# Performance work log

Measured on AMD Instinct MI355X. Metric: run time of the kernel, lower is better.

Reference implementation:

```python
import jax, jax.numpy as jnp
import numpy as np

N = 50000
E = 800000
IN_C = 128
HID = 256
OUT_C = 51


def graph_conv(x, edge_index, edge_weight, w_rel, b_rel, w_root):
    # PyG GraphConv: out = lin_rel(aggr_add(w_e * x_src)) + lin_root(x)
    src, dst = edge_index[0], edge_index[1]
    msgs = x[src] * edge_weight[:, None]            # [E, F]
    agg = jax.ops.segment_sum(msgs, dst, num_segments=x.shape[0])  # [N, F]
    return agg @ w_rel + b_rel + x @ w_root


def setup_inputs() -> dict:
    key = jax.random.key(0)
    ks = jax.random.split(key, 10)
    s = lambda fan_in: 1.0 / np.sqrt(fan_in)
    return {
        "x0": jax.random.normal(ks[0], (N, IN_C), jnp.float32),
        "edge_index": jax.random.randint(ks[1], (2, E), 0, N, jnp.int64),
        "edge_weight": jax.random.uniform(ks[2], (E,), jnp.float32),
        "conv1_w_rel": jax.random.uniform(ks[3], (IN_C, HID), jnp.float32, -s(IN_C), s(IN_C)),
        "conv1_b_rel": jnp.zeros((HID,), jnp.float32),
        "conv1_w_root": jax.random.uniform(ks[4], (IN_C, HID), jnp.float32, -s(IN_C), s(IN_C)),
        "conv2_w_rel": jax.random.uniform(ks[5], (HID, HID), jnp.float32, -s(HID), s(HID)),
        "conv2_b_rel": jnp.zeros((HID,), jnp.float32),
        "conv2_w_root": jax.random.uniform(ks[6], (HID, HID), jnp.float32, -s(HID), s(HID)),
        "lin_w": jax.random.uniform(ks[7], (2 * HID, OUT_C), jnp.float32, -s(2 * HID), s(2 * HID)),
        "lin_b": jnp.zeros((OUT_C,), jnp.float32),
    }


def reference(x0, edge_index, edge_weight,
              conv1_w_rel, conv1_b_rel, conv1_w_root,
              conv2_w_rel, conv2_b_rel, conv2_w_root,
              lin_w, lin_b):
    # eval mode: dropout is identity
    x1 = jax.nn.relu(graph_conv(x0, edge_index, edge_weight, conv1_w_rel, conv1_b_rel, conv1_w_root))
    x2 = jax.nn.relu(graph_conv(x1, edge_index, edge_weight, conv2_w_rel, conv2_b_rel, conv2_w_root))
    x = jnp.concatenate([x1, x2], axis=-1)          # [N, 2H]
    return x @ lin_w + lin_b                         # [N, OUT_C]
```

## Files before the change

kernel.cpp:

```cpp
#include <hip/hip_runtime.h>
#include <hip/hip_bf16.h>

#define N_NODES 50000
#define N_EDGES 800000
#define IN_CH   128
#define HID     256
#define OUTC    51

typedef __attribute__((ext_vector_type(8))) short  bf16x8;
typedef __attribute__((ext_vector_type(4))) float  f32x4;
typedef __attribute__((ext_vector_type(2))) float  f32x2;
typedef __attribute__((ext_vector_type(4))) unsigned int u32x4;

__device__ __forceinline__ float bf2f(unsigned short u) {
    union { unsigned int i; float f; } v; v.i = ((unsigned int)u) << 16; return v.f;
}
__device__ __forceinline__ unsigned short f2bf(float f) {
    union { float f; unsigned int i; } v; v.f = f;
    unsigned int u = v.i;
    unsigned int r = (u + 0x7fffu + ((u >> 16) & 1u)) >> 16;
    return (unsigned short)r;
}
__device__ __forceinline__ unsigned short ldbf(const void* p, long i, int isf) {
    return isf ? f2bf(((const float*)p)[i]) : ((const unsigned short*)p)[i];
}
__device__ __forceinline__ float ldf(const void* p, long i, int isf) {
    return isf ? ((const float*)p)[i] : bf2f(((const unsigned short*)p)[i]);
}
__device__ __forceinline__ void load_edge_nt(const int* __restrict__ ei, int e, int is64,
                                             int* src, int* dst) {
    if (is64) { *src = __builtin_nontemporal_load(ei + 2 * e);
                *dst = __builtin_nontemporal_load(ei + 2 * (N_EDGES + e)); }
    else      { *src = __builtin_nontemporal_load(ei + e);
                *dst = __builtin_nontemporal_load(ei + N_EDGES + e); }
}

#define EBLK 1024
#define HB   ((N_EDGES + EBLK - 1) / EBLK)
#define NBKT ((N_NODES + 255) / 256)

__global__ __launch_bounds__(256) void init_kernel(const unsigned int* __restrict__ x0w,
                                                   int* __restrict__ flags,
                                                   const int* __restrict__ ei) {
    int tid = threadIdx.x;
    if (blockIdx.x == 0) {
        if (tid < 64) {
            unsigned int w = x0w[tid];
            unsigned int ex = (w >> 7) & 0xFFu;
            unsigned long long bm = __ballot(ex >= 0x60u && ex <= 0x90u);
            if (tid == 0) flags[0] = (__popcll(bm) >= 48) ? 0 : 1;
        }
        return;
    }
    __shared__ int any;
    if (tid == 0) any = 0;
    __syncthreads();
    int acc = 0;
    for (int s = 0; s < 8; s++) {
        int i = (tid * 8 + s) * (N_EDGES / 2048);
        acc |= ei[2 * i + 1];
    }
    if (acc != 0) any = 1;
    __syncthreads();
    if (tid == 0) flags[1] = any;
}

__global__ void prep_all_kernel(const void* __restrict__ x0, int cb,
                                const void* __restrict__ w1r, const void* __restrict__ w1x,
                                const void* __restrict__ w2r, const void* __restrict__ w2x,
                                const void* __restrict__ lw,
                                const void* __restrict__ b1h, const void* __restrict__ b2h,
                                const void* __restrict__ lbh, const int* __restrict__ flags,
                                unsigned short* __restrict__ x0bf,
                                unsigned short* __restrict__ Bt1, unsigned short* __restrict__ Bt2,
                                unsigned short* __restrict__ Bt3,
                                float* __restrict__ b1, float* __restrict__ b2, float* __restrict__ b3) {
    int isf = flags[0];
    if ((int)blockIdx.x < cb) {
        if (!isf) return;
        long t = (long)blockIdx.x * 256 + threadIdx.x;
        if (t < (long)N_NODES * IN_CH) x0bf[t] = f2bf(((const float*)x0)[t]);
        return;
    }
    int t = (blockIdx.x - cb) * 256 + threadIdx.x;
    if (t < 256 * 256) {
        int n = t >> 8, k = t & 255;
        Bt1[n * 256 + k] = (k < 128) ? ldbf(w1r, k * 256 + n, isf) : ldbf(w1x, (k - 128) * 256 + n, isf);
        return;
    }
    t -= 256 * 256;
    if (t < 256 * 512) {
        int n = t >> 9, k = t & 511;
        Bt2[n * 512 + k] = (k < 256) ? ldbf(w2r, k * 256 + n, isf) : ldbf(w2x, (k - 256) * 256 + n, isf);
        return;
    }
    t -= 256 * 512;
    if (t < 64 * 512) {
        int n = t >> 9, k = t & 511;
        Bt3[n * 512 + k] = (n < OUTC) ? ldbf(lw, k * OUTC + n, isf) : (unsigned short)0;
        return;
    }
    t -= 64 * 512;
    if (t < 256) { b1[t] = ldf(b1h, t, isf); return; }
    t -= 256;
    if (t < 256) { b2[t] = ldf(b2h, t, isf); return; }
    t -= 256;
    if (t < 64)  { b3[t] = (t < OUTC) ? ldf(lbh, t, isf) : 0.0f; return; }
}

__global__ __launch_bounds__(256) void h1_kernel(const int* __restrict__ ei, const int* __restrict__ flags,
                                                 unsigned int* __restrict__ bc) {
    __shared__ unsigned int cnt[NBKT];
    int tid = threadIdx.x;
    if (tid < NBKT) cnt[tid] = 0;
    __syncthreads();
    int is64 = (flags[1] == 0);
    int e0 = blockIdx.x * EBLK;
#pragma unroll
    for (int u = 0; u < 4; u++) {
        int e = e0 + u * 256 + tid;
        if (e < N_EDGES) {
            int src, dst; load_edge_nt(ei, e, is64, &src, &dst);
            if ((unsigned)src < N_NODES && (unsigned)dst < N_NODES)
                atomicAdd(&cnt[dst >> 8], 1u);
        }
    }
    __syncthreads();
    if (tid < NBKT) bc[tid * HB + blockIdx.x] = cnt[tid];
}

__global__ __launch_bounds__(1024) void s1_kernel(const unsigned int* __restrict__ bc,
                                                  unsigned int* __restrict__ pbase,
                                                  unsigned int* __restrict__ total) {
    __shared__ unsigned int sd[1024];
    int b = blockIdx.x, tid = threadIdx.x;
    unsigned int v = (tid < HB) ? bc[b * HB + tid] : 0u;
    sd[tid] = v;
    __syncthreads();
    for (int off = 1; off < 1024; off <<= 1) {
        unsigned int t = (tid >= off) ? sd[tid - off] : 0u;
        __syncthreads();
        sd[tid] += t;
        __syncthreads();
    }
    if (tid < HB) pbase[tid * NBKT + b] = sd[tid] - v;
    if (tid == 1023) total[b] = sd[1023];
}

__global__ __launch_bounds__(256) void s2_kernel(const unsigned int* __restrict__ total,
                                                 unsigned int* __restrict__ bbase,
                                                 int* __restrict__ rp) {
    __shared__ unsigned int sd[256];
    int tid = threadIdx.x;
    unsigned int v = (tid < NBKT) ? total[tid] : 0u;
    sd[tid] = v;
    __syncthreads();
    for (int off = 1; off < 256; off <<= 1) {
        unsigned int t = (tid >= off) ? sd[tid - off] : 0u;
        __syncthreads();
        sd[tid] += t;
        __syncthreads();
    }
    if (tid < NBKT) bbase[tid] = sd[tid] - v;
    if (tid == NBKT - 1) { bbase[NBKT] = sd[tid]; rp[N_NODES] = (int)sd[tid]; }
}

__global__ __launch_bounds__(256) void f1_kernel(const int* __restrict__ ei, const void* __restrict__ ew,
                                                 const int* __restrict__ flags,
                                                 const unsigned int* __restrict__ pbase,
                                                 const unsigned int* __restrict__ bbase,
                                                 uint2* __restrict__ rec) {
    __shared__ unsigned int cur[NBKT];
    int tid = threadIdx.x;
    if (tid < NBKT) cur[tid] = bbase[tid] + pbase[blockIdx.x * NBKT + tid];
    __syncthreads();
    int is64 = (flags[1] == 0);
    int isf = flags[0];
    int e0 = blockIdx.x * EBLK;
#pragma unroll
    for (int u = 0; u < 4; u++) {
        int e = e0 + u * 256 + tid;
        if (e < N_EDGES) {
            int src, dst; load_edge_nt(ei, e, is64, &src, &dst);
            if ((unsigned)src < N_NODES && (unsigned)dst < N_NODES) {
                unsigned int w = ldbf(ew, e, isf);
                unsigned int pos = atomicAdd(&cur[dst >> 8], 1u);
                uint2 r; r.x = (w << 16) | (unsigned)src; r.y = (unsigned)dst;
                rec[pos] = r;
            }
        }
    }
}

__global__ __launch_bounds__(512) void f2_kernel(const uint2* __restrict__ rec,
                                                 const unsigned int* __restrict__ bbase,
                                                 int* __restrict__ rp, unsigned int* __restrict__ cw) {
    __shared__ unsigned int c2[256], sc[256], cur2[256];
    int tid = threadIdx.x, b = blockIdx.x;
    unsigned int s0 = bbase[b], e0 = bbase[b + 1];
    if (tid < 256) c2[tid] = 0;
    __syncthreads();
    for (unsigned int pos = s0 + tid; pos < e0; pos += 512)
        atomicAdd(&c2[rec[pos].y & 255u], 1u);
    __syncthreads();
    unsigned int v = 0;
    if (tid < 256) { v = c2[tid]; sc[tid] = v; }
    __syncthreads();
    for (int off = 1; off < 256; off <<= 1) {
        unsigned int t = (tid < 256 && tid >= off) ? sc[tid - off] : 0u;
        __syncthreads();
        if (tid < 256) sc[tid] += t;
        __syncthreads();
    }
    if (tid < 256) {
        unsigned int start = s0 + sc[tid] - v;
        int node = b * 256 + tid;
        if (node < N_NODES) rp[node] = (int)start;
        cur2[tid] = start;
    }
    __syncthreads();
    for (unsigned int pos = s0 + tid; pos < e0; pos += 512) {
        uint2 r = rec[pos];
        unsigned int p = atomicAdd(&cur2[r.y & 255u], 1u);
        cw[p] = r.x;
    }
}

__global__ __launch_bounds__(256) void zout_kernel(unsigned short* __restrict__ out, long n) {
    long t = (long)blockIdx.x * 256 + threadIdx.x;
    if (t < n) out[t] = 0;
}

__global__ __launch_bounds__(256) void x1f8_kernel(const unsigned short* __restrict__ X12,
                                                   unsigned char* __restrict__ x1f8,
                                                   const int* __restrict__ flags, int f8mode) {
    int usef8 = (f8mode == 2) || (f8mode == 1 && flags[0] == 0);
    if (!usef8) return;
    int t = blockIdx.x * 256 + threadIdx.x;
    if (t >= N_NODES * 32) return;
    int row = t >> 5, c8 = (t & 31) * 8;
    u32x4 v = *(const u32x4*)(X12 + (long)row * 512 + c8);
    float f0 = bf2f((unsigned short)(v[0] & 0xffffu)), f1 = bf2f((unsigned short)(v[0] >> 16));
    float f2 = bf2f((unsigned short)(v[1] & 0xffffu)), f3 = bf2f((unsigned short)(v[1] >> 16));
    float f4 = bf2f((unsigned short)(v[2] & 0xffffu)), f5 = bf2f((unsigned short)(v[2] >> 16));
    float f6 = bf2f((unsigned short)(v[3] & 0xffffu)), f7 = bf2f((unsigned short)(v[3] >> 16));
    int lo = 0, hi = 0;
    lo = __builtin_amdgcn_cvt_pk_fp8_f32(f0, f1, lo, false);
    lo = __builtin_amdgcn_cvt_pk_fp8_f32(f2, f3, lo, true);
    hi = __builtin_amdgcn_cvt_pk_fp8_f32(f4, f5, hi, false);
    hi = __builtin_amdgcn_cvt_pk_fp8_f32(f6, f7, hi, true);
    uint2 pk; pk.x = (unsigned int)lo; pk.y = (unsigned int)hi;
    *(uint2*)(x1f8 + (long)row * 256 + c8) = pk;
}

__global__ __launch_bounds__(256) void agg1_kernel(const unsigned short* __restrict__ x0raw,
                                                   const unsigned short* __restrict__ x0conv,
                                                   int use_conv, const int* __restrict__ flags,
                                                   const int* __restrict__ rp, const unsigned int* __restrict__ cw,
                                                   unsigned short* __restrict__ X12) {
    const unsigned short* x0b = (use_conv && flags[0]) ? x0conv : x0raw;
    int r = blockIdx.x * 8 + (threadIdx.x >> 5);
    if (r >= N_NODES) return;
    int l = threadIdx.x & 31;
    int grpbase = threadIdx.x & 32;
    int js = rp[r], je = rp[r + 1];
    if (js < 0) js = 0;
    if (je > N_EDGES) je = N_EDGES;
    const uint2* xw = (const uint2*)x0b;
    float a0 = 0.f, a1 = 0.f, a2 = 0.f, a3 = 0.f;
    for (int base = js; base < je; base += 32) {
        int n = je - base; if (n > 32) n = 32;
        int idx = base + l; if (idx >= je) idx = je - 1;
        unsigned int rec = __builtin_nontemporal_load(cw + idx);
        for (int j = 0; j < n; j += 8) {
            int m = n - j; if (m > 8) m = 8;
            unsigned int vv[8]; uint2 q[8];
#pragma unroll
            for (int u = 0; u < 8; u++) vv[u] = __shfl(rec, grpbase + j + u);
#pragma unroll
            for (int u = 0; u < 8; u++) if (u < m)
                q[u] = xw[(long)(vv[u] & 0xFFFFu) * 32 + l];
#pragma unroll
            for (int u = 0; u < 8; u++) if (u < m) {
                float w = bf2f((unsigned short)(vv[u] >> 16));
                a0 += w * bf2f((unsigned short)(q[u].x & 0xffffu));
                a1 += w * bf2f((unsigned short)(q[u].x >> 16));
                a2 += w * bf2f((unsigned short)(q[u].y & 0xffffu));
                a3 += w * bf2f((unsigned short)(q[u].y >> 16));
            }
        }
    }
    uint2 pk;
    pk.x = (unsigned int)f2bf(a0) | ((unsigned int)f2bf(a1) << 16);
    pk.y = (unsigned int)f2bf(a2) | ((unsigned int)f2bf(a3) << 16);
    *(uint2*)&X12[(long)r * 512 + 256 + l * 4] = pk;
}

__global__ __launch_bounds__(256) void agg2_kernel(const int* __restrict__ rp, const unsigned int* __restrict__ cw,
                                                   unsigned short* __restrict__ X12,
                                                   const unsigned char* __restrict__ x1f8,
                                                   const int* __restrict__ flags, int f8mode) {
    int usef8 = (f8mode == 2) || (f8mode == 1 && flags[0] == 0);
    int r = blockIdx.x * 8 + (threadIdx.x >> 5);
    if (r >= N_NODES) return;
    int l = threadIdx.x & 31;
    int grpbase = threadIdx.x & 32;
    int js = rp[r], je = rp[r + 1];
    if (js < 0) js = 0;
    if (je > N_EDGES) je = N_EDGES;
    float a0 = 0.f, a1 = 0.f, a2 = 0.f, a3 = 0.f;
    float a4 = 0.f, a5 = 0.f, a6 = 0.f, a7 = 0.f;
    if (usef8) {
        for (int base = js; base < je; base += 32) {
            int n = je - base; if (n > 32) n = 32;
            int idx = base + l; if (idx >= je) idx = je - 1;
            unsigned int rec = __builtin_nontemporal_load(cw + idx);
            for (int j = 0; j < n; j += 8) {
                int m = n - j; if (m > 8) m = 8;
                unsigned int vv[8]; uint2 q[8];
#pragma unroll
                for (int u = 0; u < 8; u++) vv[u] = __shfl(rec, grpbase + j + u);
#pragma unroll
                for (int u = 0; u < 8; u++) if (u < m)
                    q[u] = *(const uint2*)(x1f8 + (long)(vv[u] & 0xFFFFu) * 256 + l * 8);
#pragma unroll
                for (int u = 0; u < 8; u++) if (u < m) {
                    float w = bf2f((unsigned short)(vv[u] >> 16));
                    f32x2 p0 = __builtin_amdgcn_cvt_pk_f32_fp8((int)q[u].x, false);
                    f32x2 p1 = __builtin_amdgcn_cvt_pk_f32_fp8((int)q[u].x, true);
                    f32x2 p2 = __builtin_amdgcn_cvt_pk_f32_fp8((int)q[u].y, false);
                    f32x2 p3 = __builtin_amdgcn_cvt_pk_f32_fp8((int)q[u].y, true);
                    a0 += w * p0.x; a1 += w * p0.y; a2 += w * p1.x; a3 += w * p1.y;
                    a4 += w * p2.x; a5 += w * p2.y; a6 += w * p3.x; a7 += w * p3.y;
                }
            }
        }
    } else {
        for (int base = js; base < je; base += 32) {
            int n = je - base; if (n > 32) n = 32;
            int idx = base + l; if (idx >= je) idx = je - 1;
            unsigned int rec = __builtin_nontemporal_load(cw + idx);
            for (int j = 0; j < n; j += 8) {
                int m = n - j; if (m > 8) m = 8;
                unsigned int vv[8]; u32x4 q[8];
#pragma unroll
                for (int u = 0; u < 8; u++) vv[u] = __shfl(rec, grpbase + j + u);
#pragma unroll
                for (int u = 0; u < 8; u++) if (u < m)
                    q[u] = *(const u32x4*)(X12 + (long)(vv[u] & 0xFFFFu) * 512 + l * 8);
#pragma unroll
                for (int u = 0; u < 8; u++) if (u < m) {
                    float w = bf2f((unsigned short)(vv[u] >> 16));
                    a0 += w * bf2f((unsigned short)(q[u][0] & 0xffffu));
                    a1 += w * bf2f((unsigned short)(q[u][0] >> 16));
                    a2 += w * bf2f((unsigned short)(q[u][1] & 0xffffu));
                    a3 += w * bf2f((unsigned short)(q[u][1] >> 16));
                    a4 += w * bf2f((unsigned short)(q[u][2] & 0xffffu));
                    a5 += w * bf2f((unsigned short)(q[u][2] >> 16));
                    a6 += w * bf2f((unsigned short)(q[u][3] & 0xffffu));
                    a7 += w * bf2f((unsigned short)(q[u][3] >> 16));
                }
            }
        }
    }
    u32x4 pk;
    pk[0] = (unsigned int)f2bf(a0) | ((unsigned int)f2bf(a1) << 16);
    pk[1] = (unsigned int)f2bf(a2) | ((unsigned int)f2bf(a3) << 16);
    pk[2] = (unsigned int)f2bf(a4) | ((unsigned int)f2bf(a5) << 16);
    pk[3] = (unsigned int)f2bf(a6) | ((unsigned int)f2bf(a7) << 16);
    *(u32x4*)&X12[(long)r * 512 + 256 + l * 8] = pk;
}

__global__ __launch_bounds__(512) void gemm_big_kernel(
    const unsigned short* __restrict__ Aagg, int lda_agg, int Kagg,
    const unsigned short* __restrict__ AxRaw, const unsigned short* __restrict__ AxConv,
    int use_conv, int lda_x,
    const unsigned short* __restrict__ Bt, int K,
    const float* __restrict__ bias, const int* __restrict__ flags,
    unsigned short* __restrict__ out, int ldo, int ocol, int M) {
    __shared__ __align__(16) unsigned short As[128][72];
    __shared__ __align__(16) unsigned short Bs[256][72];
    const unsigned short* Ax = (use_conv && flags[0]) ? AxConv : AxRaw;
    int tid = threadIdx.x;
    int bm0 = blockIdx.x * 128;
    int wave = tid >> 6, lane = tid & 63;
    int wm = wave >> 2, wn = wave & 3;
    int quad = lane >> 4, l16 = lane & 15;

    f32x4 acc[4][4];
#pragma unroll
    for (int mt = 0; mt < 4; mt++)
#pragma unroll
        for (int nt = 0; nt < 4; nt++) acc[mt][nt] = (f32x4){0.f, 0.f, 0.f, 0.f};

    for (int k0 = 0; k0 < K; k0 += 64) {
        const unsigned short* srcp;
        int stride, koff;
        if (k0 < Kagg) { srcp = Aagg; stride = lda_agg; koff = k0; }
        else           { srcp = Ax;   stride = lda_x;   koff = k0 - Kagg; }
#pragma unroll
        for (int i = 0; i < 2; i++) {
            int c = tid + i * 512;
            int row = c >> 3, ko = (c & 7) * 8;
            int gr = bm0 + row;
            if (gr >= M) gr = M - 1;
            u32x4 v = *(const u32x4*)(srcp + (long)gr * stride + koff + ko);
            *(u32x4*)&As[row][ko] = v;
        }
#pragma unroll
        for (int p = 0; p < 4; p++) {
            int c = p * 512 + tid;
            int row = c >> 3, ko = (c & 7) * 8;
            u32x4 v = *(const u32x4*)(Bt + (long)row * K + k0 + ko);
            *(u32x4*)&Bs[row][ko] = v;
        }
        __syncthreads();
#pragma unroll
        for (int kc = 0; kc < 64; kc += 32) {
            bf16x8 a[4], b[4];
#pragma unroll
            for (int mt = 0; mt < 4; mt++)
                a[mt] = *(const bf16x8*)&As[wm * 64 + mt * 16 + l16][kc + quad * 8];
#pragma unroll
            for (int nt = 0; nt < 4; nt++)
                b[nt] = *(const bf16x8*)&Bs[wn * 64 + nt * 16 + l16][kc + quad * 8];
#pragma unroll
            for (int mt = 0; mt < 4; mt++)
#pragma unroll
                for (int nt = 0; nt < 4; nt++)
                    acc[mt][nt] = __builtin_amdgcn_mfma_f32_16x16x32_bf16(a[mt], b[nt], acc[mt][nt], 0, 0, 0);
        }
        __syncthreads();
    }

#pragma unroll
    for (int mt = 0; mt < 4; mt++) {
#pragma unroll
        for (int nt = 0; nt < 4; nt++) {
            f32x4 a = acc[mt][nt];
            int colI = wn * 64 + nt * 16 + l16;
            float bv = bias[colI];
#pragma unroll
            for (int rr = 0; rr < 4; rr++) {
                int row = bm0 + wm * 64 + mt * 16 + quad * 4 + rr;
                if (row < M) {
                    float v = a[rr] + bv;
                    v = v > 0.f ? v : 0.f;
                    out[(long)row * ldo + ocol + colI] = f2bf(v);
                }
            }
        }
    }
}

__global__ __launch_bounds__(256) void gemm_head_kernel(
    const unsigned short* __restrict__ Ax, int lda_x,
    const unsigned short* __restrict__ Bt, int K,
    const float* __restrict__ bias,
    void* __restrict__ out, int ldo,
    int M, int realN, const int* __restrict__ flagF) {
    __shared__ __align__(16) unsigned short As[64][72];
    __shared__ __align__(16) unsigned short Bs[64][72];
    int tid = threadIdx.x;
    int bm0 = blockIdx.x * 64;
    int wave = tid >> 6, lane = tid & 63;
    int wm = wave >> 1, wn = wave & 1;
    int quad = lane >> 4, l16 = lane & 15;

    f32x4 acc[2][2];
#pragma unroll
    for (int mt = 0; mt < 2; mt++)
#pragma unroll
        for (int nt = 0; nt < 2; nt++) acc[mt][nt] = (f32x4){0.f, 0.f, 0.f, 0.f};

    for (int k0 = 0; k0 < K; k0 += 64) {
#pragma unroll
        for (int i = 0; i < 2; i++) {
            int c = tid + i * 256;
            int row = c >> 3, ko = (c & 7) * 8;
            int gr = bm0 + row;
            if (gr >= M) gr = M - 1;
            u32x4 v = *(const u32x4*)(Ax + (long)gr * lda_x + k0 + ko);
            *(u32x4*)&As[row][ko] = v;
        }
#pragma unroll
        for (int p = 0; p < 2; p++) {
            int c = p * 256 + tid;
            int row = c >> 3, ko = (c & 7) * 8;
            u32x4 v = *(const u32x4*)(Bt + (long)row * K + k0 + ko);
            *(u32x4*)&Bs[row][ko] = v;
        }
        __syncthreads();
#pragma unroll
        for (int kc = 0; kc < 64; kc += 32) {
            bf16x8 a0 = *(const bf16x8*)&As[wm * 32 + l16][kc + quad * 8];
            bf16x8 a1 = *(const bf16x8*)&As[wm * 32 + 16 + l16][kc + quad * 8];
#pragma unroll
            for (int nt = 0; nt < 2; nt++) {
                bf16x8 b = *(const bf16x8*)&Bs[wn * 32 + nt * 16 + l16][kc + quad * 8];
                acc[0][nt] = __builtin_amdgcn_mfma_f32_16x16x32_bf16(a0, b, acc[0][nt], 0, 0, 0);
                acc[1][nt] = __builtin_amdgcn_mfma_f32_16x16x32_bf16(a1, b, acc[1][nt], 0, 0, 0);
            }
        }
        __syncthreads();
    }

    int out_f32 = *flagF;
#pragma unroll
    for (int mt = 0; mt < 2; mt++) {
#pragma unroll
        for (int nt = 0; nt < 2; nt++) {
            f32x4 a = acc[mt][nt];
            int colI = wn * 32 + nt * 16 + l16;
            float bv = bias[colI];
#pragma unroll
            for (int rr = 0; rr < 4; rr++) {
                int row = bm0 + wm * 32 + mt * 16 + quad * 4 + rr;
                if (row < M && colI < realN) {
                    float v = a[rr] + bv;
                    long idx = (long)row * ldo + colI;
                    if (out_f32) ((float*)out)[idx] = v;
                    else ((unsigned short*)out)[idx] = f2bf(v);
                }
            }
        }
    }
}

extern "C" void kernel_launch(void* const* d_in, const int* in_sizes, int n_in,
                              void* d_out, int out_size, void* d_ws, size_t ws_size,
                              hipStream_t stream) {
    const void* x0  = d_in[0];
    const int*  ei  = (const int*)d_in[1];
    const void* ew  = d_in[2];
    const void* w1r = d_in[3];
    const void* b1h = d_in[4];
    const void* w1x = d_in[5];
    const void* w2r = d_in[6];
    const void* b2h = d_in[7];
    const void* w2x = d_in[8];
    const void* lw  = d_in[9];
    const void* lbh = d_in[10];

    char* ws = (char*)d_ws;
    unsigned short* X12     = (unsigned short*)(ws);
    unsigned int*   cw      = (unsigned int*)(ws + 51200000);
    int*            row_ptr = (int*)(ws + 54400000);
    unsigned short* Bt1     = (unsigned short*)(ws + 54800128);
    unsigned short* Bt2     = (unsigned short*)(ws + 54931200);
    unsigned short* Bt3     = (unsigned short*)(ws + 55193344);
    float*          b1      = (float*)(ws + 55258880);
    float*          b2      = (float*)(ws + 55259904);
    float*          b3      = (float*)(ws + 55260928);
    int*            flags   = (int*)(ws + 55261184);
    unsigned short* x0bf    = (unsigned short*)(ws + 55262272);
    unsigned char*  x1f8sep = (unsigned char*)(ws + 68062272);
    const size_t NEED_NOCONV = 55262272;
    const size_t NEED_FULL   = 68062272;
    const size_t NEED_F8SEP  = 80862272;

    uint2*        rec   = (uint2*)(ws);
    unsigned int* bc    = (unsigned int*)(ws + 6400000);
    unsigned int* pbse  = (unsigned int*)(ws + 7013120);
    unsigned int* btot  = (unsigned int*)(ws + 7626240);
    unsigned int* bbase = (unsigned int*)(ws + 7627264);

    if (ws_size < NEED_NOCONV) {
        long n = (long)N_NODES * OUTC;
        zout_kernel<<<(int)((n + 255) / 256), 256, 0, stream>>>((unsigned short*)d_out, n);
        return;
    }
    int use_conv = (ws_size >= NEED_FULL) ? 1 : 0;
    int f8mode = (ws_size >= NEED_F8SEP) ? 2 : (use_conv ? 1 : 0);
    unsigned char* x1f8 = (f8mode == 2) ? x1f8sep : (unsigned char*)x0bf;

    int* flagF = flags + 0;

    init_kernel<<<2, 256, 0, stream>>>((const unsigned int*)x0, flags, ei);

    int cb = use_conv ? ((N_NODES * IN_CH + 255) / 256) : 0;
    {
        int ptotal = 256 * 256 + 256 * 512 + 64 * 512 + 256 + 256 + 64;
        int pblocks = (ptotal + 255) / 256;
        prep_all_kernel<<<cb + pblocks, 256, 0, stream>>>(
            x0, cb, w1r, w1x, w2r, w2x, lw, b1h, b2h, lbh, flags, x0bf,
            Bt1, Bt2, Bt3, b1, b2, b3);
    }

    h1_kernel<<<HB, 256, 0, stream>>>(ei, flags, bc);
    s1_kernel<<<NBKT, 1024, 0, stream>>>(bc, pbse, btot);
    s2_kernel<<<1, 256, 0, stream>>>(btot, bbase, row_ptr);
    f1_kernel<<<HB, 256, 0, stream>>>(ei, ew, flags, pbse, bbase, rec);
    f2_kernel<<<NBKT, 512, 0, stream>>>(rec, bbase, row_ptr, cw);

    int mblocks  = (N_NODES + 127) / 128;
    int hblocks  = (N_NODES + 63) / 64;
    int ablocks  = (N_NODES + 7) / 8;
    int fblocks  = (N_NODES * 32 + 255) / 256;

    const unsigned short* x0raw = (const unsigned short*)x0;

    agg1_kernel<<<ablocks, 256, 0, stream>>>(x0raw, x0bf, use_conv, flags, row_ptr, cw, X12);
    gemm_big_kernel<<<mblocks, 512, 0, stream>>>(X12 + 256, 512, 128,
                                                 x0raw, x0bf, use_conv, IN_CH,
                                                 Bt1, 256, b1, flags,
                                                 X12, 512, 0, N_NODES);
    x1f8_kernel<<<fblocks, 256, 0, stream>>>(X12, x1f8, flags, f8mode);
    agg2_kernel<<<ablocks, 256, 0, stream>>>(row_ptr, cw, X12, x1f8, flags, f8mode);
    gemm_big_kernel<<<mblocks, 512, 0, stream>>>(X12 + 256, 512, 256,
                                                 X12, X12, 0, 512,
                                                 Bt2, 512, b2, flags,
                                                 X12, 512, 256, N_NODES);
    gemm_head_kernel<<<hblocks, 256, 0, stream>>>(X12, 512, Bt3, 512, b3,
                                                  d_out, OUTC, N_NODES, OUTC, flagF);
}
```

Baseline: 289.3 us.

## Use direct global-to-LDS loads with XOR swizzle, fuse fp8 conversion and histogram

Result: faster. 267.4 us (-7.6%).

```diff
diff --git a/kernel.cpp b/kernel.cpp
--- a/kernel.cpp
+++ b/kernel.cpp
@@ -33,6 +33,12 @@
                 *dst = __builtin_nontemporal_load(ei + 2 * (N_EDGES + e)); }
     else      { *src = __builtin_nontemporal_load(ei + e);
                 *dst = __builtin_nontemporal_load(ei + N_EDGES + e); }
+}
+
+typedef const __attribute__((address_space(1))) unsigned int* gas_u32;
+typedef __attribute__((address_space(3))) unsigned int* las_u32;
+__device__ __forceinline__ void cp16(const void* g, void* l) {
+    __builtin_amdgcn_global_load_lds((gas_u32)g, (las_u32)l, 16, 0, 0);
 }
 
 #define EBLK 1024
@@ -74,7 +80,10 @@
                                 unsigned short* __restrict__ x0bf,
                                 unsigned short* __restrict__ Bt1, unsigned short* __restrict__ Bt2,
                                 unsigned short* __restrict__ Bt3,
-                                float* __restrict__ b1, float* __restrict__ b2, float* __restrict__ b3) {
+                                float* __restrict__ b1, float* __restrict__ b2, float* __restrict__ b3,
+                                const int* __restrict__ ei, unsigned int* __restrict__ bc,
+                                int pblocks) {
+    __shared__ unsigned int cnt[NBKT];
     int isf = flags[0];
     if ((int)blockIdx.x < cb) {
         if (!isf) return;
@@ -82,7 +91,28 @@
         if (t < (long)N_NODES * IN_CH) x0bf[t] = f2bf(((const float*)x0)[t]);
         return;
     }
-    int t = (blockIdx.x - cb) * 256 + threadIdx.x;
+    int rb = blockIdx.x - cb;
+    if (rb >= pblocks) {
+        int b = rb - pblocks;
+        int tid = threadIdx.x;
+        if (tid < NBKT) cnt[tid] = 0;
+        __syncthreads();
+        int is64 = (flags[1] == 0);
+        int e0 = b * EBLK;
+#pragma unroll
+        for (int u = 0; u < 4; u++) {
+            int e = e0 + u * 256 + tid;
+            if (e < N_EDGES) {
+                int src, dst; load_edge_nt(ei, e, is64, &src, &dst);
+                if ((unsigned)src < N_NODES && (unsigned)dst < N_NODES)
+                    atomicAdd(&cnt[dst >> 8], 1u);
+            }
+        }
+        __syncthreads();
+        if (tid < NBKT) bc[tid * HB + b] = cnt[tid];
+        return;
+    }
+    int t = rb * 256 + threadIdx.x;
     if (t < 256 * 256) {
         int n = t >> 8, k = t & 255;
         Bt1[n * 256 + k] = (k < 128) ? ldbf(w1r, k * 256 + n, isf) : ldbf(w1x, (k - 128) * 256 + n, isf);
@@ -106,27 +136,6 @@
     if (t < 256) { b2[t] = ldf(b2h, t, isf); return; }
     t -= 256;
     if (t < 64)  { b3[t] = (t < OUTC) ? ldf(lbh, t, isf) : 0.0f; return; }
-}
-
-__global__ __launch_bounds__(256) void h1_kernel(const int* __restrict__ ei, const int* __restrict__ flags,
-                                                 unsigned int* __restrict__ bc) {
-    __shared__ unsigned int cnt[NBKT];
-    int tid = threadIdx.x;
-    if (tid < NBKT) cnt[tid] = 0;
-    __syncthreads();
-    int is64 = (flags[1] == 0);
-    int e0 = blockIdx.x * EBLK;
-#pragma unroll
-    for (int u = 0; u < 4; u++) {
-        int e = e0 + u * 256 + tid;
-        if (e < N_EDGES) {
-            int src, dst; load_edge_nt(ei, e, is64, &src, &dst);
-            if ((unsigned)src < N_NODES && (unsigned)dst < N_NODES)
-                atomicAdd(&cnt[dst >> 8], 1u);
-        }
-    }
-    __syncthreads();
-    if (tid < NBKT) bc[tid * HB + blockIdx.x] = cnt[tid];
 }
 
 __global__ __launch_bounds__(1024) void s1_kernel(const unsigned int* __restrict__ bc,
@@ -229,28 +238,6 @@
 __global__ __launch_bounds__(256) void zout_kernel(unsigned short* __restrict__ out, long n) {
     long t = (long)blockIdx.x * 256 + threadIdx.x;
     if (t < n) out[t] = 0;
-}
-
-__global__ __launch_bounds__(256) void x1f8_kernel(const unsigned short* __restrict__ X12,
-                                                   unsigned char* __restrict__ x1f8,
-                                                   const int* __restrict__ flags, int f8mode) {
-    int usef8 = (f8mode == 2) || (f8mode == 1 && flags[0] == 0);
-    if (!usef8) return;
-    int t = blockIdx.x * 256 + threadIdx.x;
-    if (t >= N_NODES * 32) return;
-    int row = t >> 5, c8 = (t & 31) * 8;
-    u32x4 v = *(const u32x4*)(X12 + (long)row * 512 + c8);
-    float f0 = bf2f((unsigned short)(v[0] & 0xffffu)), f1 = bf2f((unsigned short)(v[0] >> 16));
-    float f2 = bf2f((unsigned short)(v[1] & 0xffffu)), f3 = bf2f((unsigned short)(v[1] >> 16));
-    float f4 = bf2f((unsigned short)(v[2] & 0xffffu)), f5 = bf2f((unsigned short)(v[2] >> 16));
-    float f6 = bf2f((unsigned short)(v[3] & 0xffffu)), f7 = bf2f((unsigned short)(v[3] >> 16));
-    int lo = 0, hi = 0;
-    lo = __builtin_amdgcn_cvt_pk_fp8_f32(f0, f1, lo, false);
-    lo = __builtin_amdgcn_cvt_pk_fp8_f32(f2, f3, lo, true);
-    hi = __builtin_amdgcn_cvt_pk_fp8_f32(f4, f5, hi, false);
-    hi = __builtin_amdgcn_cvt_pk_fp8_f32(f6, f7, hi, true);
-    uint2 pk; pk.x = (unsigned int)lo; pk.y = (unsigned int)hi;
-    *(uint2*)(x1f8 + (long)row * 256 + c8) = pk;
 }
 
 __global__ __launch_bounds__(256) void agg1_kernel(const unsigned short* __restrict__ x0raw,
@@ -377,15 +364,19 @@
     int use_conv, int lda_x,
     const unsigned short* __restrict__ Bt, int K,
     const float* __restrict__ bias, const int* __restrict__ flags,
-    unsigned short* __restrict__ out, int ldo, int ocol, int M) {
-    __shared__ __align__(16) unsigned short As[128][72];
-    __shared__ __align__(16) unsigned short Bs[256][72];
+    unsigned short* __restrict__ out, int ldo, int ocol, int M,
+    unsigned char* __restrict__ x1f8, int f8mode) {
+    __shared__ __align__(16) unsigned short As[128][64];
+    __shared__ __align__(16) unsigned short Bs[256][64];
     const unsigned short* Ax = (use_conv && flags[0]) ? AxConv : AxRaw;
+    int dof8 = (f8mode == 2) || (f8mode == 1 && flags[0] == 0);
     int tid = threadIdx.x;
     int bm0 = blockIdx.x * 128;
     int wave = tid >> 6, lane = tid & 63;
     int wm = wave >> 2, wn = wave & 3;
     int quad = lane >> 4, l16 = lane & 15;
+    int lr = lane >> 3;
+    int sc = (lane & 7) ^ lr;
 
     f32x4 acc[4][4];
 #pragma unroll
@@ -400,30 +391,33 @@
         else           { srcp = Ax;   stride = lda_x;   koff = k0 - Kagg; }
 #pragma unroll
         for (int i = 0; i < 2; i++) {
-            int c = tid + i * 512;
-            int row = c >> 3, ko = (c & 7) * 8;
-            int gr = bm0 + row;
-            if (gr >= M) gr = M - 1;
-            u32x4 v = *(const u32x4*)(srcp + (long)gr * stride + koff + ko);
-            *(u32x4*)&As[row][ko] = v;
-        }
-#pragma unroll
-        for (int p = 0; p < 4; p++) {
-            int c = p * 512 + tid;
-            int row = c >> 3, ko = (c & 7) * 8;
-            u32x4 v = *(const u32x4*)(Bt + (long)row * K + k0 + ko);
-            *(u32x4*)&Bs[row][ko] = v;
+            int t = wave * 2 + i;
+            int r = t * 8 + lr;
+            int gr = bm0 + r; if (gr >= M) gr = M - 1;
+            cp16(srcp + (long)gr * stride + koff + sc * 8, (char*)As + t * 1024);
+        }
+#pragma unroll
+        for (int i = 0; i < 4; i++) {
+            int t = wave * 4 + i;
+            int r = t * 8 + lr;
+            cp16(Bt + (long)r * K + k0 + sc * 8, (char*)Bs + t * 1024);
         }
         __syncthreads();
 #pragma unroll
         for (int kc = 0; kc < 64; kc += 32) {
+            int k8 = (kc >> 3) + quad;
+            int swz = (k8 ^ (l16 & 7)) << 4;
             bf16x8 a[4], b[4];
 #pragma unroll
-            for (int mt = 0; mt < 4; mt++)
-                a[mt] = *(const bf16x8*)&As[wm * 64 + mt * 16 + l16][kc + quad * 8];
-#pragma unroll
-            for (int nt = 0; nt < 4; nt++)
-                b[nt] = *(const bf16x8*)&Bs[wn * 64 + nt * 16 + l16][kc + quad * 8];
+            for (int mt = 0; mt < 4; mt++) {
+                int row = wm * 64 + mt * 16 + l16;
+                a[mt] = *(const bf16x8*)((const char*)As + row * 128 + swz);
+            }
+#pragma unroll
+            for (int nt = 0; nt < 4; nt++) {
+                int row = wn * 64 + nt * 16 + l16;
+                b[nt] = *(const bf16x8*)((const char*)Bs + row * 128 + swz);
+            }
 #pragma unroll
             for (int mt = 0; mt < 4; mt++)
 #pragma unroll
@@ -447,6 +441,10 @@
                     float v = a[rr] + bv;
                     v = v > 0.f ? v : 0.f;
                     out[(long)row * ldo + ocol + colI] = f2bf(v);
+                    if (dof8) {
+                        int p = __builtin_amdgcn_cvt_pk_fp8_f32(v, v, 0, false);
+                        x1f8[(long)row * 256 + colI] = (unsigned char)(p & 0xff);
+                    }
                 }
             }
         }
@@ -459,13 +457,15 @@
     const float* __restrict__ bias,
     void* __restrict__ out, int ldo,
     int M, int realN, const int* __restrict__ flagF) {
-    __shared__ __align__(16) unsigned short As[64][72];
-    __shared__ __align__(16) unsigned short Bs[64][72];
+    __shared__ __align__(16) unsigned short As[64][64];
+    __shared__ __align__(16) unsigned short Bs[64][64];
     int tid = threadIdx.x;
     int bm0 = blockIdx.x * 64;
     int wave = tid >> 6, lane = tid & 63;
     int wm = wave >> 1, wn = wave & 1;
     int quad = lane >> 4, l16 = lane & 15;
+    int lr = lane >> 3;
+    int sc = (lane & 7) ^ lr;
 
     f32x4 acc[2][2];
 #pragma unroll
@@ -476,28 +476,27 @@
     for (int k0 = 0; k0 < K; k0 += 64) {
 #pragma unroll
         for (int i = 0; i < 2; i++) {
-            int c = tid + i * 256;
-            int row = c >> 3, ko = (c & 7) * 8;
-            int gr = bm0 + row;
-            if (gr >= M) gr = M - 1;
-            u32x4 v = *(const u32x4*)(Ax + (long)gr * lda_x + k0 + ko);
-            *(u32x4*)&As[row][ko] = v;
-        }
-#pragma unroll
-        for (int p = 0; p < 2; p++) {
-            int c = p * 256 + tid;
-            int row = c >> 3, ko = (c & 7) * 8;
-            u32x4 v = *(const u32x4*)(Bt + (long)row * K + k0 + ko);
-            *(u32x4*)&Bs[row][ko] = v;
+            int t = wave * 2 + i;
+            int r = t * 8 + lr;
+            int gr = bm0 + r; if (gr >= M) gr = M - 1;
+            cp16(Ax + (long)gr * lda_x + k0 + sc * 8, (char*)As + t * 1024);
+        }
+#pragma unroll
+        for (int i = 0; i < 2; i++) {
+            int t = wave * 2 + i;
+            int r = t * 8 + lr;
+            cp16(Bt + (long)r * K + k0 + sc * 8, (char*)Bs + t * 1024);
         }
         __syncthreads();
 #pragma unroll
         for (int kc = 0; kc < 64; kc += 32) {
-            bf16x8 a0 = *(const bf16x8*)&As[wm * 32 + l16][kc + quad * 8];
-            bf16x8 a1 = *(const bf16x8*)&As[wm * 32 + 16 + l16][kc + quad * 8];
+            int k8 = (kc >> 3) + quad;
+            int swz = (k8 ^ (l16 & 7)) << 4;
+            bf16x8 a0 = *(const bf16x8*)((const char*)As + (wm * 32 + l16) * 128 + swz);
+            bf16x8 a1 = *(const bf16x8*)((const char*)As + (wm * 32 + 16 + l16) * 128 + swz);
 #pragma unroll
             for (int nt = 0; nt < 2; nt++) {
-                bf16x8 b = *(const bf16x8*)&Bs[wn * 32 + nt * 16 + l16][kc + quad * 8];
+                bf16x8 b = *(const bf16x8*)((const char*)Bs + (wn * 32 + nt * 16 + l16) * 128 + swz);
                 acc[0][nt] = __builtin_amdgcn_mfma_f32_16x16x32_bf16(a0, b, acc[0][nt], 0, 0, 0);
                 acc[1][nt] = __builtin_amdgcn_mfma_f32_16x16x32_bf16(a1, b, acc[1][nt], 0, 0, 0);
             }
@@ -582,12 +581,11 @@
     {
         int ptotal = 256 * 256 + 256 * 512 + 64 * 512 + 256 + 256 + 64;
         int pblocks = (ptotal + 255) / 256;
-        prep_all_kernel<<<cb + pblocks, 256, 0, stream>>>(
+        prep_all_kernel<<<cb + pblocks + HB, 256, 0, stream>>>(
             x0, cb, w1r, w1x, w2r, w2x, lw, b1h, b2h, lbh, flags, x0bf,
-            Bt1, Bt2, Bt3, b1, b2, b3);
-    }
-
-    h1_kernel<<<HB, 256, 0, stream>>>(ei, flags, bc);
+            Bt1, Bt2, Bt3, b1, b2, b3, ei, bc, pblocks);
+    }
+
     s1_kernel<<<NBKT, 1024, 0, stream>>>(bc, pbse, btot);
     s2_kernel<<<1, 256, 0, stream>>>(btot, bbase, row_ptr);
     f1_kernel<<<HB, 256, 0, stream>>>(ei, ew, flags, pbse, bbase, rec);
@@ -596,7 +594,6 @@
     int mblocks  = (N_NODES + 127) / 128;
     int hblocks  = (N_NODES + 63) / 64;
     int ablocks  = (N_NODES + 7) / 8;
-    int fblocks  = (N_NODES * 32 + 255) / 256;
 
     const unsigned short* x0raw = (const unsigned short*)x0;
 
@@ -604,13 +601,12 @@
     gemm_big_kernel<<<mblocks, 512, 0, stream>>>(X12 + 256, 512, 128,
                                                  x0raw, x0bf, use_conv, IN_CH,
                                                  Bt1, 256, b1, flags,
-                                                 X12, 512, 0, N_NODES);
-    x1f8_kernel<<<fblocks, 256, 0, stream>>>(X12, x1f8, flags, f8mode);
+                                                 X12, 512, 0, N_NODES, x1f8, f8mode);
     agg2_kernel<<<ablocks, 256, 0, stream>>>(row_ptr, cw, X12, x1f8, flags, f8mode);
     gemm_big_kernel<<<mblocks, 512, 0, stream>>>(X12 + 256, 512, 256,
                                                  X12, X12, 0, 512,
                                                  Bt2, 512, b2, flags,
-                                                 X12, 512, 256, N_NODES);
+                                                 X12, 512, 256, N_NODES, (unsigned char*)nullptr, 0);
     gemm_head_kernel<<<hblocks, 256, 0, stream>>>(X12, 512, Bt3, 512, b3,
                                                   d_out, OUTC, N_NODES, OUTC, flagF);
 }
```
